# Kernel optimization log

Measured on AMD Instinct MI355X. Metric: run time of the kernel, lower is better.

Reference implementation:

```python
import jax, jax.numpy as jnp
import numpy as np

B, T, U = 8, 256, 64
ENC_DIM, DEC_DIM, JOINT_DIM, VOCAB = 512, 512, 640, 1024


def setup_inputs() -> dict:
    key = jax.random.key(0)
    k1, k2, k3, k4, k5 = jax.random.split(key, 5)
    s_enc = 1.0 / np.sqrt(ENC_DIM)
    s_dec = 1.0 / np.sqrt(DEC_DIM)
    s_joint = 1.0 / np.sqrt(JOINT_DIM)
    return {
        "enc_out": jax.random.normal(k1, (B, T, ENC_DIM), dtype=jnp.float32),
        "pred_out": jax.random.normal(k2, (B, U, DEC_DIM), dtype=jnp.float32),
        # nn.Linear weights stored as [out, in], applied as x @ W.T
        "W_enc": jax.random.uniform(k3, (JOINT_DIM, ENC_DIM), jnp.float32, -s_enc, s_enc),
        "W_pred": jax.random.uniform(k4, (JOINT_DIM, DEC_DIM), jnp.float32, -s_dec, s_dec),
        "W_out": jax.random.uniform(k5, (VOCAB, JOINT_DIM), jnp.float32, -s_joint, s_joint),
    }


def reference(enc_out, pred_out, W_enc, W_pred, W_out):
    # project: [B,T,J] and [B,U,J]
    enc_p = jnp.einsum("bte,je->btj", enc_out, W_enc)
    pred_p = jnp.einsum("bud,jd->buj", pred_out, W_pred)
    # broadcast add -> [B,T,U,J], SiLU, then output GEMM -> [B,T,U,V]
    joint = enc_p[:, :, None, :] + pred_p[:, None, :, :]
    joint = joint * jax.nn.sigmoid(joint)  # SiLU
    out = jnp.einsum("btuj,vj->btuv", joint, W_out)
    return out
```

## Files before the change

kernel.cpp:

```cpp
#include <hip/hip_runtime.h>

typedef unsigned short u16;
typedef __attribute__((ext_vector_type(8))) short short8;
typedef __attribute__((ext_vector_type(8))) unsigned short ushort8v;
typedef __attribute__((ext_vector_type(4))) float f32x4;

#define B_ 8
#define T_ 256
#define U_ 64
#define E_ 512
#define J_ 640
#define V_ 1024
#define NT 20

__device__ __forceinline__ u16 f2bf(float f) {
  unsigned int u = __float_as_uint(f);
  u += 0x7fffu + ((u >> 16) & 1u);
  return (u16)(u >> 16);
}

__device__ __forceinline__ void gload16(const void* g, void* l) {
  __builtin_amdgcn_global_load_lds((const __attribute__((address_space(1))) void*)g,
                                   (__attribute__((address_space(3))) void*)l,
                                   16, 0, 0);
}

__global__ __launch_bounds__(256) void cast5_k(const float4* __restrict__ s0,
                                               const float4* __restrict__ s1,
                                               const float4* __restrict__ s2,
                                               const float4* __restrict__ s3,
                                               const float4* __restrict__ s4,
                                               ushort4* __restrict__ dst) {
  int i = blockIdx.x * 256 + threadIdx.x;
  const int st = gridDim.x * 256;
  for (; i < 655360; i += st) {
    const float4* s; int off;
    if (i < 262144)      { s = s0; off = 0; }
    else if (i < 327680) { s = s1; off = 262144; }
    else if (i < 409600) { s = s2; off = 327680; }
    else if (i < 491520) { s = s3; off = 409600; }
    else                 { s = s4; off = 491520; }
    float4 v = s[i - off];
    ushort4 o;
    o.x = f2bf(v.x); o.y = f2bf(v.y); o.z = f2bf(v.z); o.w = f2bf(v.w);
    dst[i] = o;
  }
}

__global__ __launch_bounds__(256) void proj_k(const u16* __restrict__ X,
                                              const u16* __restrict__ W,
                                              float* __restrict__ C) {
  __shared__ __align__(16) u16 As[128 * 32];
  __shared__ __align__(16) u16 Bs[128 * 32];
  const int tid = threadIdx.x;
  const int w = tid >> 6, lane = tid & 63;
  const int wr = w >> 1, wc = w & 1;
  const int m0 = blockIdx.x * 128, n0 = blockIdx.y * 128;
  const int lr = lane & 15, lk = lane >> 4;
  const int r4 = tid >> 2, kq = tid & 3;

  f32x4 acc[4][4] = {};

  for (int ks = 0; ks < E_ / 32; ++ks) {
    const int k0 = ks * 32;
    gload16(X + (size_t)(m0 + r4) * E_ + k0 + kq * 8, (char*)As + w * 1024);
    gload16(X + (size_t)(m0 + 64 + r4) * E_ + k0 + kq * 8, (char*)As + 4096 + w * 1024);
    gload16(W + (size_t)(n0 + r4) * E_ + k0 + kq * 8, (char*)Bs + w * 1024);
    gload16(W + (size_t)(n0 + 64 + r4) * E_ + k0 + kq * 8, (char*)Bs + 4096 + w * 1024);
    __syncthreads();
    short8 a[4], bb[4];
#pragma unroll
    for (int m = 0; m < 4; ++m)
      a[m] = *(const short8*)&As[(wr * 64 + m * 16 + lr) * 32 + lk * 8];
#pragma unroll
    for (int n = 0; n < 4; ++n)
      bb[n] = *(const short8*)&Bs[(wc * 64 + n * 16 + lr) * 32 + lk * 8];
#pragma unroll
    for (int m = 0; m < 4; ++m)
#pragma unroll
      for (int n = 0; n < 4; ++n)
        acc[m][n] = __builtin_amdgcn_mfma_f32_16x16x32_bf16(a[m], bb[n], acc[m][n], 0, 0, 0);
    __syncthreads();
  }

#pragma unroll
  for (int m = 0; m < 4; ++m) {
    const int row = m0 + wr * 64 + m * 16 + lk * 4;
#pragma unroll
    for (int n = 0; n < 4; ++n) {
      const int col = n0 + wc * 64 + n * 16 + lr;
#pragma unroll
      for (int i = 0; i < 4; ++i)
        C[(size_t)(row + i) * J_ + col] = acc[m][n][i];
    }
  }
}

__global__ __launch_bounds__(256) void pack_k(const u16* __restrict__ Wo,
                                              u16* __restrict__ pk) {
  const int u = blockIdx.x * 256 + threadIdx.x;
  const int l = u & 63;
  int r = u >> 6;
  const int nq = r & 3;  r >>= 2;
  const int ks = r % 20;
  const int vt = r / 20;
  const int v = vt * 64 + nq * 16 + (l & 15);
  const int k = ks * 32 + (l >> 4) * 8;
  *(short8*)(pk + (size_t)u * 8) = *(const short8*)(Wo + (size_t)v * J_ + k);
}

__global__ __launch_bounds__(1024, 1) void fused3_k(const float* __restrict__ ep,
                                                    const float* __restrict__ pp,
                                                    const u16* __restrict__ pk,
                                                    float* __restrict__ out) {
  __shared__ __align__(16) u16 Alds[64 * 640];
  const int tid = threadIdx.x;
  const int w = tid >> 6, lane = tid & 63;
  const int lr = lane & 15, lk = lane >> 4;
  const int bt = blockIdx.x;
  const int b = bt >> 8;
  const size_t m0 = (size_t)bt * 64;

  const u16* bp = pk + (size_t)w * 40960 + lane * 8;

  short8 BE[4], BO[4], a[4];

#define BL(bF, ks)                                                             \
  do {                                                                         \
    _Pragma("unroll")                                                          \
    for (int nq = 0; nq < 4; ++nq)                                             \
      bF[nq] = *(const short8*)(bp + (ks) * 2048 + nq * 512);                  \
  } while (0)

  BL(BE, 0);

  const float* eprow = ep + (size_t)bt * J_;
  const float* pbase = pp + (size_t)b * 64 * J_;
#pragma unroll
  for (int it = 0; it < 5; ++it) {
    const int unit = tid + it * 1024;
    const int row = unit / 80;
    const int c = unit - row * 80;
    union { float4 v[2]; float f[8]; } Ee, Pp;
    Ee.v[0] = *(const float4*)(eprow + c * 8);
    Ee.v[1] = *(const float4*)(eprow + c * 8 + 4);
    Pp.v[0] = *(const float4*)(pbase + (size_t)row * J_ + c * 8);
    Pp.v[1] = *(const float4*)(pbase + (size_t)row * J_ + c * 8 + 4);
    union { ushort8v v; u16 s[8]; } R;
#pragma unroll
    for (int j = 0; j < 8; ++j) {
      float x = Ee.f[j] + Pp.f[j];
      R.s[j] = f2bf(x * __builtin_amdgcn_rcpf(1.0f + __expf(-x)));
    }
    *(ushort8v*)&Alds[row * 640 + ((c ^ (row & 7)) << 3)] = R.v;
  }
  __syncthreads();

  const int rx = lr & 7;

#define AR(ks)                                                                 \
  do {                                                                         \
    _Pragma("unroll")                                                          \
    for (int mq = 0; mq < 4; ++mq)                                             \
      a[mq] = *(const short8*)&Alds[(mq * 16 + lr) * 640 +                     \
                                    ((((ks) * 4 + lk) ^ rx) << 3)];            \
  } while (0)

#define MM(bF)                                                                 \
  do {                                                                         \
    __builtin_amdgcn_s_setprio(1);                                             \
    _Pragma("unroll")                                                          \
    for (int mq = 0; mq < 4; ++mq)                                             \
      _Pragma("unroll")                                                        \
      for (int nq = 0; nq < 4; ++nq)                                           \
        acc[mq][nq] = __builtin_amdgcn_mfma_f32_16x16x32_bf16(bF[nq], a[mq],   \
                                                              acc[mq][nq], 0, 0, 0); \
    __builtin_amdgcn_s_setprio(0);                                             \
  } while (0)

  f32x4 acc[4][4] = {};

#pragma unroll 1
  for (int ks = 0; ks < NT; ks += 2) {
    AR(ks);
    BL(BO, ks + 1);
    MM(BE);
    __builtin_amdgcn_sched_barrier(0);
    AR(ks + 1);
    if (ks + 2 < NT) BL(BE, ks + 2);
    MM(BO);
    __builtin_amdgcn_sched_barrier(0);
  }

#pragma unroll
  for (int mq = 0; mq < 4; ++mq) {
    const size_t row = m0 + mq * 16 + lr;
#pragma unroll
    for (int nq = 0; nq < 4; ++nq) {
      const int col = w * 64 + nq * 16 + lk * 4;
      *(float4*)&out[row * V_ + col] = *(float4*)&acc[mq][nq];
    }
  }
#undef AR
#undef BL
#undef MM
}

extern "C" void kernel_launch(void* const* d_in, const int* in_sizes, int n_in,
                              void* d_out, int out_size, void* d_ws, size_t ws_size,
                              hipStream_t stream) {
  const float* enc = (const float*)d_in[0];
  const float* pred = (const float*)d_in[1];
  const float* We = (const float*)d_in[2];
  const float* Wp = (const float*)d_in[3];
  const float* Wo = (const float*)d_in[4];
  float* out = (float*)d_out;

  char* ws = (char*)d_ws;
  u16* enc_bf = (u16*)ws;
  u16* pred_bf = (u16*)(ws + 2097152);
  u16* We_bf = (u16*)(ws + 2621440);
  u16* Wp_bf = (u16*)(ws + 3276800);
  u16* Wo_bf = (u16*)(ws + 3932160);
  float* ep = (float*)(ws + 5242880);
  float* pp = (float*)(ws + 10485760);
  u16* Wo_pk = (u16*)(ws + 11796480);

  cast5_k<<<2048, 256, 0, stream>>>((const float4*)enc, (const float4*)pred,
                                    (const float4*)We, (const float4*)Wp,
                                    (const float4*)Wo, (ushort4*)ws);

  proj_k<<<dim3(16, 5), 256, 0, stream>>>(enc_bf, We_bf, ep);
  proj_k<<<dim3(4, 5), 256, 0, stream>>>(pred_bf, Wp_bf, pp);
  pack_k<<<320, 256, 0, stream>>>(Wo_bf, Wo_pk);

  fused3_k<<<2048, 1024, 0, stream>>>(ep, pp, Wo_pk, out);
}
```

Measured before the change: 249.7 us.

## Halve LDS tile and block size, loop K in halves with two output tiles per wave

```diff
diff --git a/kernel.cpp b/kernel.cpp
--- a/kernel.cpp
+++ b/kernel.cpp
@@ -11,7 +11,6 @@
 #define E_ 512
 #define J_ 640
 #define V_ 1024
-#define NT 20
 
 __device__ __forceinline__ u16 f2bf(float f) {
   unsigned int u = __float_as_uint(f);
@@ -109,101 +108,130 @@
   *(short8*)(pk + (size_t)u * 8) = *(const short8*)(Wo + (size_t)v * J_ + k);
 }
 
-__global__ __launch_bounds__(1024, 1) void fused3_k(const float* __restrict__ ep,
-                                                    const float* __restrict__ pp,
-                                                    const u16* __restrict__ pk,
-                                                    float* __restrict__ out) {
-  __shared__ __align__(16) u16 Alds[64 * 640];
+__global__ __launch_bounds__(512, 4) void fused5_k(const float* __restrict__ ep,
+                                                   const float* __restrict__ pp,
+                                                   const u16* __restrict__ pk,
+                                                   float* __restrict__ out) {
+  __shared__ __align__(16) u16 Alds[64 * 320];
   const int tid = threadIdx.x;
   const int w = tid >> 6, lane = tid & 63;
   const int lr = lane & 15, lk = lane >> 4;
   const int bt = blockIdx.x;
   const int b = bt >> 8;
   const size_t m0 = (size_t)bt * 64;
-
-  const u16* bp = pk + (size_t)w * 40960 + lane * 8;
-
-  short8 BE[4], BO[4], a[4];
-
-#define BL(bF, ks)                                                             \
-  do {                                                                         \
-    _Pragma("unroll")                                                          \
-    for (int nq = 0; nq < 4; ++nq)                                             \
-      bF[nq] = *(const short8*)(bp + (ks) * 2048 + nq * 512);                  \
-  } while (0)
-
-  BL(BE, 0);
+  const int rx = lr & 7;
+
+  const u16* bp0 = pk + (size_t)(2 * w) * 40960 + lane * 8;
+  const u16* bp1 = bp0 + 40960;
 
   const float* eprow = ep + (size_t)bt * J_;
   const float* pbase = pp + (size_t)b * 64 * J_;
-#pragma unroll
-  for (int it = 0; it < 5; ++it) {
-    const int unit = tid + it * 1024;
-    const int row = unit / 80;
-    const int c = unit - row * 80;
-    union { float4 v[2]; float f[8]; } Ee, Pp;
-    Ee.v[0] = *(const float4*)(eprow + c * 8);
-    Ee.v[1] = *(const float4*)(eprow + c * 8 + 4);
-    Pp.v[0] = *(const float4*)(pbase + (size_t)row * J_ + c * 8);
-    Pp.v[1] = *(const float4*)(pbase + (size_t)row * J_ + c * 8 + 4);
-    union { ushort8v v; u16 s[8]; } R;
-#pragma unroll
-    for (int j = 0; j < 8; ++j) {
-      float x = Ee.f[j] + Pp.f[j];
-      R.s[j] = f2bf(x * __builtin_amdgcn_rcpf(1.0f + __expf(-x)));
-    }
-    *(ushort8v*)&Alds[row * 640 + ((c ^ (row & 7)) << 3)] = R.v;
-  }
-  __syncthreads();
-
-  const int rx = lr & 7;
-
-#define AR(ks)                                                                 \
+
+  short8 BE[4], BO[4], a[4];
+
+#define BL(bF, bp, ks)                                                         \
+  do {                                                                         \
+    _Pragma("unroll")                                                          \
+    for (int nq = 0; nq < 4; ++nq)                                             \
+      bF[nq] = *(const short8*)((bp) + (ks) * 2048 + nq * 512);                \
+  } while (0)
+
+#define BUILD(h)                                                               \
+  do {                                                                         \
+    _Pragma("unroll")                                                          \
+    for (int it = 0; it < 5; ++it) {                                           \
+      const int unit = tid + it * 512;       \
+      const int row = unit / 40;                                               \
+      const int c = unit - row * 40;                                           \
+      const int kg = (h) * 320 + c * 8;                                        \
+      union { float4 v[2]; float f[8]; } Ee, Pp;                               \
+      Ee.v[0] = *(const float4*)(eprow + kg);                                  \
+      Ee.v[1] = *(const float4*)(eprow + kg + 4);                              \
+      Pp.v[0] = *(const float4*)(pbase + (size_t)row * J_ + kg);               \
+      Pp.v[1] = *(const float4*)(pbase + (size_t)row * J_ + kg + 4);           \
+      union { ushort8v v; u16 s[8]; } R;                                       \
+      _Pragma("unroll")                                                        \
+      for (int j = 0; j < 8; ++j) {                                            \
+        float x = Ee.f[j] + Pp.f[j];                                           \
+        R.s[j] = f2bf(x * __builtin_amdgcn_rcpf(1.0f + __expf(-x)));           \
+      }                                                                        \
+      *(ushort8v*)&Alds[row * 320 + ((c ^ (row & 7)) << 3)] = R.v;             \
+    }                                                                          \
+  } while (0)
+
+#define AR(ksl)                                                                \
   do {                                                                         \
     _Pragma("unroll")                                                          \
     for (int mq = 0; mq < 4; ++mq)                                             \
-      a[mq] = *(const short8*)&Alds[(mq * 16 + lr) * 640 +                     \
-                                    ((((ks) * 4 + lk) ^ rx) << 3)];            \
-  } while (0)
-
-#define MM(bF)                                                                 \
-  do {                                                                         \
-    __builtin_amdgcn_s_setprio(1);                                             \
+      a[mq] = *(const short8*)&Alds[(mq * 16 + lr) * 320 +                     \
+                                    ((((ksl) * 4 + lk) ^ rx) << 3)];           \
+  } while (0)
+
+#define MM(bF, acc)                                                            \
+  do {                                                                         \
     _Pragma("unroll")                                                          \
     for (int mq = 0; mq < 4; ++mq)                                             \
       _Pragma("unroll")                                                        \
       for (int nq = 0; nq < 4; ++nq)                                           \
         acc[mq][nq] = __builtin_amdgcn_mfma_f32_16x16x32_bf16(bF[nq], a[mq],   \
                                                               acc[mq][nq], 0, 0, 0); \
-    __builtin_amdgcn_s_setprio(0);                                             \
-  } while (0)
-
-  f32x4 acc[4][4] = {};
-
-#pragma unroll 1
-  for (int ks = 0; ks < NT; ks += 2) {
-    AR(ks);
-    BL(BO, ks + 1);
-    MM(BE);
-    __builtin_amdgcn_sched_barrier(0);
-    AR(ks + 1);
-    if (ks + 2 < NT) BL(BE, ks + 2);
-    MM(BO);
-    __builtin_amdgcn_sched_barrier(0);
-  }
-
-#pragma unroll
-  for (int mq = 0; mq < 4; ++mq) {
-    const size_t row = m0 + mq * 16 + lr;
-#pragma unroll
-    for (int nq = 0; nq < 4; ++nq) {
-      const int col = w * 64 + nq * 16 + lk * 4;
-      *(float4*)&out[row * V_ + col] = *(float4*)&acc[mq][nq];
-    }
-  }
+  } while (0)
+
+#define KLOOP10(bp, ks0, acc, bpn, ksn)                                        \
+  do {                                                                         \
+    _Pragma("unroll")                                                          \
+    for (int it = 0; it < 5; ++it) {                                           \
+      BL(BO, bp, (ks0) + 2 * it + 1);                                          \
+      AR(2 * it);                                                              \
+      MM(BE, acc);                                                             \
+      if (it < 4) BL(BE, bp, (ks0) + 2 * it + 2);                              \
+      else        BL(BE, bpn, ksn);                                            \
+      AR(2 * it + 1);                                                          \
+      MM(BO, acc);                                                             \
+    }                                                                          \
+  } while (0)
+
+#define STORE(acc, vtc)                                                        \
+  do {                                                                         \
+    _Pragma("unroll")                                                          \
+    for (int mq = 0; mq < 4; ++mq) {                                           \
+      const size_t row = m0 + mq * 16 + lr;                                    \
+      _Pragma("unroll")                                                        \
+      for (int nq = 0; nq < 4; ++nq) {                                         \
+        const int col = (vtc) * 64 + nq * 16 + lk * 4;                         \
+        *(float4*)&out[row * V_ + col] = *(float4*)&acc[mq][nq];               \
+      }                                                                        \
+    }                                                                          \
+  } while (0)
+
+  BL(BE, bp0, 0);
+  BUILD(0);
+  __syncthreads();
+
+  {
+    f32x4 acc0[4][4] = {};
+    KLOOP10(bp0, 0, acc0, bp0, 10);
+    __syncthreads();
+    BUILD(1);
+    __syncthreads();
+    KLOOP10(bp0, 10, acc0, bp1, 10);
+    STORE(acc0, 2 * w);
+  }
+  {
+    f32x4 acc1[4][4] = {};
+    KLOOP10(bp1, 10, acc1, bp1, 0);
+    __syncthreads();
+    BUILD(0);
+    __syncthreads();
+    KLOOP10(bp1, 0, acc1, bp1, 0);
+    STORE(acc1, 2 * w + 1);
+  }
+#undef BL
+#undef BUILD
 #undef AR
-#undef BL
 #undef MM
+#undef KLOOP10
+#undef STORE
 }
 
 extern "C" void kernel_launch(void* const* d_in, const int* in_sizes, int n_in,
@@ -234,5 +262,5 @@
   proj_k<<<dim3(4, 5), 256, 0, stream>>>(pred_bf, Wp_bf, pp);
   pack_k<<<320, 256, 0, stream>>>(Wo_bf, Wo_pk);
 
-  fused3_k<<<2048, 1024, 0, stream>>>(ep, pp, Wo_pk, out);
-}
+  fused5_k<<<2048, 512, 0, stream>>>(ep, pp, Wo_pk, out);
+}
```

Result: slower. 788.8 us (+215.9%).

## Process two 64-row tiles per block with 8 waves looping over vocab halves

Applied to the files above, without the earlier changes.

```diff
diff --git a/kernel.cpp b/kernel.cpp
--- a/kernel.cpp
+++ b/kernel.cpp
@@ -109,101 +109,132 @@
   *(short8*)(pk + (size_t)u * 8) = *(const short8*)(Wo + (size_t)v * J_ + k);
 }
 
-__global__ __launch_bounds__(1024, 1) void fused3_k(const float* __restrict__ ep,
-                                                    const float* __restrict__ pp,
-                                                    const u16* __restrict__ pk,
-                                                    float* __restrict__ out) {
-  __shared__ __align__(16) u16 Alds[64 * 640];
+__global__ __launch_bounds__(512, 2) void fused6_k(const float* __restrict__ ep,
+                                                   const float* __restrict__ pp,
+                                                   const u16* __restrict__ pk,
+                                                   float* __restrict__ out) {
+  __shared__ __align__(16) u16 Alds[2][64 * 640];
   const int tid = threadIdx.x;
   const int w = tid >> 6, lane = tid & 63;
   const int lr = lane & 15, lk = lane >> 4;
-  const int bt = blockIdx.x;
-  const int b = bt >> 8;
-  const size_t m0 = (size_t)bt * 64;
-
-  const u16* bp = pk + (size_t)w * 40960 + lane * 8;
-
-  short8 BE[4], BO[4], a[4];
-
-#define BL(bF, ks)                                                             \
+  const int bt0 = blockIdx.x * 2;
+  const int b = bt0 >> 8;
+  const size_t m00 = (size_t)bt0 * 64;
+  const int rx = lr & 7;
+
+  const u16* bpA = pk + (size_t)w * 40960 + lane * 8;
+  const u16* bpB = pk + (size_t)(w + 8) * 40960 + lane * 8;
+
+  const float* ep0 = ep + (size_t)bt0 * J_;
+  const float* pbase = pp + (size_t)b * 64 * J_;
+
+  short8 BE[4], BO[4], a0[4], a1[4];
+
+#define BL(bF, bp, ks)                                                         \
   do {                                                                         \
     _Pragma("unroll")                                                          \
     for (int nq = 0; nq < 4; ++nq)                                             \
-      bF[nq] = *(const short8*)(bp + (ks) * 2048 + nq * 512);                  \
-  } while (0)
-
-  BL(BE, 0);
-
-  const float* eprow = ep + (size_t)bt * J_;
-  const float* pbase = pp + (size_t)b * 64 * J_;
-#pragma unroll
-  for (int it = 0; it < 5; ++it) {
-    const int unit = tid + it * 1024;
-    const int row = unit / 80;
-    const int c = unit - row * 80;
+      bF[nq] = *(const short8*)((bp) + (ks) * 2048 + nq * 512);                \
+  } while (0)
+
+  BL(BE, bpA, 0);
+
+#pragma unroll
+  for (int it = 0; it < 20; ++it) {
+    const int unit = tid + it * 512;
+    const int pnl = unit >= 5120;
+    const int u2 = unit - pnl * 5120;
+    const int row = u2 / 80;
+    const int c = u2 - row * 80;
+    const float* er = ep0 + pnl * J_ + c * 8;
+    const float* pr = pbase + (size_t)row * J_ + c * 8;
     union { float4 v[2]; float f[8]; } Ee, Pp;
-    Ee.v[0] = *(const float4*)(eprow + c * 8);
-    Ee.v[1] = *(const float4*)(eprow + c * 8 + 4);
-    Pp.v[0] = *(const float4*)(pbase + (size_t)row * J_ + c * 8);
-    Pp.v[1] = *(const float4*)(pbase + (size_t)row * J_ + c * 8 + 4);
+    Ee.v[0] = *(const float4*)er;       Ee.v[1] = *(const float4*)(er + 4);
+    Pp.v[0] = *(const float4*)pr;       Pp.v[1] = *(const float4*)(pr + 4);
     union { ushort8v v; u16 s[8]; } R;
 #pragma unroll
     for (int j = 0; j < 8; ++j) {
       float x = Ee.f[j] + Pp.f[j];
       R.s[j] = f2bf(x * __builtin_amdgcn_rcpf(1.0f + __expf(-x)));
     }
-    *(ushort8v*)&Alds[row * 640 + ((c ^ (row & 7)) << 3)] = R.v;
+    *(ushort8v*)&Alds[pnl][row * 640 + ((c ^ (row & 7)) << 3)] = R.v;
   }
   __syncthreads();
 
-  const int rx = lr & 7;
-
-#define AR(ks)                                                                 \
-  do {                                                                         \
-    _Pragma("unroll")                                                          \
-    for (int mq = 0; mq < 4; ++mq)                                             \
-      a[mq] = *(const short8*)&Alds[(mq * 16 + lr) * 640 +                     \
-                                    ((((ks) * 4 + lk) ^ rx) << 3)];            \
-  } while (0)
-
-#define MM(bF)                                                                 \
+#define AR2(ks)                                                                \
+  do {                                                                         \
+    _Pragma("unroll")                                                          \
+    for (int mq = 0; mq < 4; ++mq) {                                           \
+      const int off = (mq * 16 + lr) * 640 + ((((ks) * 4 + lk) ^ rx) << 3);    \
+      a0[mq] = *(const short8*)&Alds[0][off];                                  \
+      a1[mq] = *(const short8*)&Alds[1][off];                                  \
+    }                                                                          \
+  } while (0)
+
+#define MM2(bF)                                                                \
   do {                                                                         \
     __builtin_amdgcn_s_setprio(1);                                             \
     _Pragma("unroll")                                                          \
     for (int mq = 0; mq < 4; ++mq)                                             \
       _Pragma("unroll")                                                        \
-      for (int nq = 0; nq < 4; ++nq)                                           \
-        acc[mq][nq] = __builtin_amdgcn_mfma_f32_16x16x32_bf16(bF[nq], a[mq],   \
-                                                              acc[mq][nq], 0, 0, 0); \
+      for (int nq = 0; nq < 4; ++nq) {                                         \
+        acc0[mq][nq] = __builtin_amdgcn_mfma_f32_16x16x32_bf16(bF[nq], a0[mq], \
+                                                               acc0[mq][nq], 0, 0, 0); \
+        acc1[mq][nq] = __builtin_amdgcn_mfma_f32_16x16x32_bf16(bF[nq], a1[mq], \
+                                                               acc1[mq][nq], 0, 0, 0); \
+      }                                                                        \
     __builtin_amdgcn_s_setprio(0);                                             \
   } while (0)
 
-  f32x4 acc[4][4] = {};
-
+#define STORE2(vtc)                                                            \
+  do {                                                                         \
+    _Pragma("unroll")                                                          \
+    for (int mq = 0; mq < 4; ++mq) {                                           \
+      const size_t r0 = m00 + mq * 16 + lr;                                    \
+      _Pragma("unroll")                                                        \
+      for (int nq = 0; nq < 4; ++nq) {                                         \
+        const int col = (vtc) * 64 + nq * 16 + lk * 4;                         \
+        *(float4*)&out[r0 * V_ + col] = *(float4*)&acc0[mq][nq];               \
+        *(float4*)&out[(r0 + 64) * V_ + col] = *(float4*)&acc1[mq][nq];        \
+      }                                                                        \
+    }                                                                          \
+  } while (0)
+
+  {
+    f32x4 acc0[4][4] = {}, acc1[4][4] = {};
 #pragma unroll 1
-  for (int ks = 0; ks < NT; ks += 2) {
-    AR(ks);
-    BL(BO, ks + 1);
-    MM(BE);
-    __builtin_amdgcn_sched_barrier(0);
-    AR(ks + 1);
-    if (ks + 2 < NT) BL(BE, ks + 2);
-    MM(BO);
-    __builtin_amdgcn_sched_barrier(0);
-  }
-
-#pragma unroll
-  for (int mq = 0; mq < 4; ++mq) {
-    const size_t row = m0 + mq * 16 + lr;
-#pragma unroll
-    for (int nq = 0; nq < 4; ++nq) {
-      const int col = w * 64 + nq * 16 + lk * 4;
-      *(float4*)&out[row * V_ + col] = *(float4*)&acc[mq][nq];
-    }
-  }
-#undef AR
+    for (int it = 0; it < NT / 2; ++it) {
+      BL(BO, bpA, 2 * it + 1);
+      AR2(2 * it);
+      MM2(BE);
+      __builtin_amdgcn_sched_barrier(0);
+      if (it < NT / 2 - 1) BL(BE, bpA, 2 * it + 2);
+      else                 BL(BE, bpB, 0);
+      AR2(2 * it + 1);
+      MM2(BO);
+      __builtin_amdgcn_sched_barrier(0);
+    }
+    STORE2(w);
+  }
+  {
+    f32x4 acc0[4][4] = {}, acc1[4][4] = {};
+#pragma unroll 1
+    for (int it = 0; it < NT / 2; ++it) {
+      BL(BO, bpB, 2 * it + 1);
+      AR2(2 * it);
+      MM2(BE);
+      __builtin_amdgcn_sched_barrier(0);
+      if (it < NT / 2 - 1) BL(BE, bpB, 2 * it + 2);
+      AR2(2 * it + 1);
+      MM2(BO);
+      __builtin_amdgcn_sched_barrier(0);
+    }
+    STORE2(w + 8);
+  }
 #undef BL
-#undef MM
+#undef AR2
+#undef MM2
+#undef STORE2
 }
 
 extern "C" void kernel_launch(void* const* d_in, const int* in_sizes, int n_in,
@@ -234,5 +265,5 @@
   proj_k<<<dim3(4, 5), 256, 0, stream>>>(pred_bf, Wp_bf, pp);
   pack_k<<<320, 256, 0, stream>>>(Wo_bf, Wo_pk);
 
-  fused3_k<<<2048, 1024, 0, stream>>>(ep, pp, Wo_pk, out);
-}
+  fused6_k<<<1024, 512, 0, stream>>>(ep, pp, Wo_pk, out);
+}
```

Result: faster. 242.0 us (-3.1%).

## Make fused joint kernel persistent with double-buffered A tile and overlapped stores

Applied to the files above, without the earlier changes.

```diff
diff --git a/kernel.cpp b/kernel.cpp
--- a/kernel.cpp
+++ b/kernel.cpp
@@ -109,101 +109,163 @@
   *(short8*)(pk + (size_t)u * 8) = *(const short8*)(Wo + (size_t)v * J_ + k);
 }
 
-__global__ __launch_bounds__(1024, 1) void fused3_k(const float* __restrict__ ep,
-                                                    const float* __restrict__ pp,
-                                                    const u16* __restrict__ pk,
-                                                    float* __restrict__ out) {
-  __shared__ __align__(16) u16 Alds[64 * 640];
+__global__ __launch_bounds__(512, 2) void fused7_k(const float* __restrict__ ep,
+                                                   const float* __restrict__ pp,
+                                                   const u16* __restrict__ pk,
+                                                   float* __restrict__ out) {
+  __shared__ __align__(16) u16 Alds[2][64 * 640];
   const int tid = threadIdx.x;
   const int w = tid >> 6, lane = tid & 63;
   const int lr = lane & 15, lk = lane >> 4;
-  const int bt = blockIdx.x;
-  const int b = bt >> 8;
-  const size_t m0 = (size_t)bt * 64;
-
-  const u16* bp = pk + (size_t)w * 40960 + lane * 8;
+  const int rx = lr & 7;
+  const int bt0 = blockIdx.x * 8;
+  const int b = bt0 >> 8;
+
+  const u16* bpA = pk + (size_t)w * 40960 + lane * 8;
+  const u16* bpB = pk + (size_t)(w + 8) * 40960 + lane * 8;
+  const float* pbase = pp + (size_t)b * 64 * J_;
 
   short8 BE[4], BO[4], a[4];
-
-#define BL(bF, ks)                                                             \
+  union F8 { float4 v[2]; float f[8]; } bEe, bPp;
+  f32x4 accA[4][4], accB[4][4];
+
+#define BL(bF, bp, ks)                                                         \
   do {                                                                         \
     _Pragma("unroll")                                                          \
     for (int nq = 0; nq < 4; ++nq)                                             \
-      bF[nq] = *(const short8*)(bp + (ks) * 2048 + nq * 512);                  \
-  } while (0)
-
-  BL(BE, 0);
-
-  const float* eprow = ep + (size_t)bt * J_;
-  const float* pbase = pp + (size_t)b * 64 * J_;
-#pragma unroll
-  for (int it = 0; it < 5; ++it) {
-    const int unit = tid + it * 1024;
-    const int row = unit / 80;
-    const int c = unit - row * 80;
-    union { float4 v[2]; float f[8]; } Ee, Pp;
-    Ee.v[0] = *(const float4*)(eprow + c * 8);
-    Ee.v[1] = *(const float4*)(eprow + c * 8 + 4);
-    Pp.v[0] = *(const float4*)(pbase + (size_t)row * J_ + c * 8);
-    Pp.v[1] = *(const float4*)(pbase + (size_t)row * J_ + c * 8 + 4);
-    union { ushort8v v; u16 s[8]; } R;
-#pragma unroll
-    for (int j = 0; j < 8; ++j) {
-      float x = Ee.f[j] + Pp.f[j];
-      R.s[j] = f2bf(x * __builtin_amdgcn_rcpf(1.0f + __expf(-x)));
-    }
-    *(ushort8v*)&Alds[row * 640 + ((c ^ (row & 7)) << 3)] = R.v;
-  }
-  __syncthreads();
-
-  const int rx = lr & 7;
-
-#define AR(ks)                                                                 \
+      bF[nq] = *(const short8*)((bp) + (ks) * 2048 + nq * 512);                \
+  } while (0)
+
+#define AR(Ap, ks)                                                             \
   do {                                                                         \
     _Pragma("unroll")                                                          \
     for (int mq = 0; mq < 4; ++mq)                                             \
-      a[mq] = *(const short8*)&Alds[(mq * 16 + lr) * 640 +                     \
+      a[mq] = *(const short8*)&(Ap)[(mq * 16 + lr) * 640 +                     \
                                     ((((ks) * 4 + lk) ^ rx) << 3)];            \
   } while (0)
 
-#define MM(bF)                                                                 \
+#define MM(bF, ACC)                                                            \
   do {                                                                         \
     __builtin_amdgcn_s_setprio(1);                                             \
     _Pragma("unroll")                                                          \
     for (int mq = 0; mq < 4; ++mq)                                             \
       _Pragma("unroll")                                                        \
       for (int nq = 0; nq < 4; ++nq)                                           \
-        acc[mq][nq] = __builtin_amdgcn_mfma_f32_16x16x32_bf16(bF[nq], a[mq],   \
-                                                              acc[mq][nq], 0, 0, 0); \
+        ACC[mq][nq] = __builtin_amdgcn_mfma_f32_16x16x32_bf16(bF[nq], a[mq],   \
+                                                              ACC[mq][nq], 0, 0, 0); \
     __builtin_amdgcn_s_setprio(0);                                             \
   } while (0)
 
-  f32x4 acc[4][4] = {};
+#define ST1(ACCP, idx, m0p, vtp)                                               \
+  do {                                                                         \
+    const int mq_ = (idx) >> 2, nq_ = (idx) & 3;                               \
+    *(float4*)&out[((m0p) + mq_ * 16 + lr) * V_ + (vtp) * 64 + nq_ * 16 + lk * 4] = \
+        *(float4*)&ACCP[mq_][nq_];                                             \
+  } while (0)
+
+#define BLD_LD(slot, epN)                                                      \
+  do {                                                                         \
+    const int u_ = tid + (slot) * 512;                                         \
+    const int row_ = u_ / 80, c_ = u_ - row_ * 80;                             \
+    bEe.v[0] = *(const float4*)((epN) + c_ * 8);                               \
+    bEe.v[1] = *(const float4*)((epN) + c_ * 8 + 4);                           \
+    bPp.v[0] = *(const float4*)(pbase + (size_t)row_ * J_ + c_ * 8);           \
+    bPp.v[1] = *(const float4*)(pbase + (size_t)row_ * J_ + c_ * 8 + 4);       \
+  } while (0)
+
+#define BLD_ST(slot, An)                                                       \
+  do {                                                                         \
+    const int u_ = tid + (slot) * 512;                                         \
+    const int row_ = u_ / 80, c_ = u_ - row_ * 80;                             \
+    union { ushort8v v; u16 s[8]; } R_;                                        \
+    _Pragma("unroll")                                                          \
+    for (int j = 0; j < 8; ++j) {                                              \
+      float x = bEe.f[j] + bPp.f[j];                                           \
+      R_.s[j] = f2bf(x * __builtin_amdgcn_rcpf(1.0f + __expf(-x)));            \
+    }                                                                          \
+    *(ushort8v*)&(An)[row_ * 640 + ((c_ ^ (row_ & 7)) << 3)] = R_.v;           \
+  } while (0)
+
+#define PASS(Ap, ACC, ACCP, doStP, m0p, vtp, bp, bpn, SB, doB, An, epN)        \
+  do {                                                                         \
+    _Pragma("unroll")                                                          \
+    for (int mq = 0; mq < 4; ++mq)                                             \
+      _Pragma("unroll")                                                        \
+      for (int nq = 0; nq < 4; ++nq)                                           \
+        ACC[mq][nq] = (f32x4){0.f, 0.f, 0.f, 0.f};                             \
+    _Pragma("unroll")                                                          \
+    for (int it = 0; it < 10; ++it) {                                          \
+      BL(BO, bp, 2 * it + 1);                                                  \
+      AR(Ap, 2 * it);                                                          \
+      MM(BE, ACC);                                                             \
+      if ((doStP) && 2 * it < 16) ST1(ACCP, 2 * it, m0p, vtp);                 \
+      if ((it & 1) == 1) {                                                     \
+        const int sl_ = (SB) + (it >> 1);                                      \
+        if (doB) {                                                             \
+          if (sl_ > 0) BLD_ST(sl_ - 1, An);                                    \
+          BLD_LD(sl_, epN);                                                    \
+        }                                                                      \
+      }                                                                        \
+      if (it < 9) BL(BE, bp, 2 * it + 2);                                      \
+      else        BL(BE, bpn, 0);                                              \
+      AR(Ap, 2 * it + 1);                                                      \
+      MM(BO, ACC);                                                             \
+      if ((doStP) && 2 * it + 1 < 16) ST1(ACCP, 2 * it + 1, m0p, vtp);         \
+      __builtin_amdgcn_sched_barrier(0);                                       \
+    }                                                                          \
+  } while (0)
+
+  BL(BE, bpA, 0);
+  {
+    const float* ep0 = ep + (size_t)bt0 * J_;
+#pragma unroll
+    for (int it = 0; it < 10; ++it) {
+      const int u_ = tid + it * 512;
+      const int row_ = u_ / 80, c_ = u_ - row_ * 80;
+      union F8 Ee, Pp;
+      Ee.v[0] = *(const float4*)(ep0 + c_ * 8);
+      Ee.v[1] = *(const float4*)(ep0 + c_ * 8 + 4);
+      Pp.v[0] = *(const float4*)(pbase + (size_t)row_ * J_ + c_ * 8);
+      Pp.v[1] = *(const float4*)(pbase + (size_t)row_ * J_ + c_ * 8 + 4);
+      union { ushort8v v; u16 s[8]; } R;
+#pragma unroll
+      for (int j = 0; j < 8; ++j) {
+        float x = Ee.f[j] + Pp.f[j];
+        R.s[j] = f2bf(x * __builtin_amdgcn_rcpf(1.0f + __expf(-x)));
+      }
+      *(ushort8v*)&Alds[0][row_ * 640 + ((c_ ^ (row_ & 7)) << 3)] = R.v;
+    }
+  }
 
 #pragma unroll 1
-  for (int ks = 0; ks < NT; ks += 2) {
-    AR(ks);
-    BL(BO, ks + 1);
-    MM(BE);
-    __builtin_amdgcn_sched_barrier(0);
-    AR(ks + 1);
-    if (ks + 2 < NT) BL(BE, ks + 2);
-    MM(BO);
-    __builtin_amdgcn_sched_barrier(0);
-  }
-
-#pragma unroll
-  for (int mq = 0; mq < 4; ++mq) {
-    const size_t row = m0 + mq * 16 + lr;
-#pragma unroll
-    for (int nq = 0; nq < 4; ++nq) {
-      const int col = w * 64 + nq * 16 + lk * 4;
-      *(float4*)&out[row * V_ + col] = *(float4*)&acc[mq][nq];
-    }
-  }
+  for (int i = 0; i < 8; ++i) {
+    const int cur = i & 1, nxt = cur ^ 1;
+    const u16* Ap = &Alds[cur][0];
+    u16* An = &Alds[nxt][0];
+    const size_t m0 = (size_t)(bt0 + i) * 64;
+    const float* epN = ep + (size_t)(bt0 + i + 1) * J_;
+    const bool doB = (i < 7);
+    const bool st0 = (i > 0);
+
+    __syncthreads();
+
+    PASS(Ap, accA, accB, st0, m0 - 64, w + 8, bpA, bpB, 0, doB, An, epN);
+    PASS(Ap, accB, accA, true, m0, w, bpB, bpA, 5, doB, An, epN);
+    if (doB) BLD_ST(9, An);
+  }
+
+  {
+    const size_t m0 = (size_t)(bt0 + 7) * 64;
+#pragma unroll
+    for (int idx = 0; idx < 16; ++idx) ST1(accB, idx, m0, w + 8);
+  }
+#undef BL
 #undef AR
-#undef BL
 #undef MM
+#undef ST1
+#undef BLD_LD
+#undef BLD_ST
+#undef PASS
 }
 
 extern "C" void kernel_launch(void* const* d_in, const int* in_sizes, int n_in,
@@ -234,5 +296,5 @@
   proj_k<<<dim3(4, 5), 256, 0, stream>>>(pred_bf, Wp_bf, pp);
   pack_k<<<320, 256, 0, stream>>>(Wo_bf, Wo_pk);
 
-  fused3_k<<<2048, 1024, 0, stream>>>(ep, pp, Wo_pk, out);
-}
+  fused7_k<<<256, 512, 0, stream>>>(ep, pp, Wo_pk, out);
+}
```

New measurement: 987.0 us. 3.95x slower.
